# Kernel optimization log

Hardware: AMD Instinct MI355X
Metric: run time of the kernel (lower is better)

Reference implementation:

```python
import jax, jax.numpy as jnp
import numpy as np

TOP_K = 8
N_GROUP = 8
TOPK_GROUP = 4
ROUTED_SCALING_FACTOR = 2.5
NORM_TOPK_PROB = True
TOKENS = 16384
HIDDEN = 4096
N_EXPERTS = 256


def setup_inputs() -> dict:
    key = jax.random.key(0)
    k1, k2, k3 = jax.random.split(key, 3)
    x = jax.random.normal(k1, (TOKENS, HIDDEN), dtype=jnp.float32)
    weight = jax.random.normal(k2, (N_EXPERTS, HIDDEN), dtype=jnp.float32) * 0.02
    e_score_correction_bias = jax.random.normal(k3, (N_EXPERTS,), dtype=jnp.float32) * 0.01
    return {"x": x, "weight": weight, "e_score_correction_bias": e_score_correction_bias}


def reference(x, weight, e_score_correction_bias):
    # gates: [T, E]
    gates = x @ weight.T
    orig_scores = jax.nn.sigmoid(gates.astype(jnp.float32))
    scores = orig_scores + e_score_correction_bias
    T, E = scores.shape
    eg = E // N_GROUP  # experts per group
    s = scores.reshape(T, N_GROUP, eg)
    # group score = sum of top-2 expert scores within each group -> [T, G]
    group_scores = jax.lax.top_k(s, 2)[0].sum(axis=-1)
    # torch code selects the (n_group - topk_group) SMALLEST groups and keeps
    # only those (masked_fill zeroes everything else) -- replicate faithfully.
    k_drop = N_GROUP - TOPK_GROUP
    _, bottom_idx = jax.lax.top_k(-group_scores, k_drop)  # [T, k_drop]
    keep = jnp.zeros((T, N_GROUP), dtype=bool).at[jnp.arange(T)[:, None], bottom_idx].set(True)
    s = jnp.where(keep[:, :, None], s, 0.0).reshape(T, E)
    # torch.topk(-scores) -> indices of the k SMALLEST scores
    _, inds = jax.lax.top_k(-s, TOP_K)  # [T, top_k]
    sel = jnp.take_along_axis(orig_scores, inds, axis=-1)
    if TOP_K > 1 and NORM_TOPK_PROB:
        sel = sel / (sel.sum(axis=-1, keepdims=True) + 1e-20)
    sel = sel * ROUTED_SCALING_FACTOR
    return inds, sel
```

## Files before the change

kernel.cpp:

```cpp
#include <hip/hip_runtime.h>
#include <hip/hip_fp16.h>
#include <cstdint>
#include <cmath>

#define TOKENS  16384
#define HIDDEN  4096
#define NEXP    256
#define TOPK    8
#define KDROP   4

typedef _Float16 f16x8  __attribute__((ext_vector_type(8)));
typedef float    f32x16 __attribute__((ext_vector_type(16)));

#define LO_SCALE 2048.0f
#define LO_INV   (1.0f/2048.0f)

#define WS_G0_OFF 0
#define WS_G1_OFF 16777216
#define WS_WH_OFF 33554432
#define WS_WL_OFF 35651584

__global__ __launch_bounds__(256)
void wsplit(const float* __restrict__ w, _Float16* __restrict__ wh,
            _Float16* __restrict__ wl)
{
    const int idx = blockIdx.x * 256 + threadIdx.x;
    const int e   = idx >> 9;
    const int kg8 = idx & 511;
    const float4* p = (const float4*)(w + (size_t)e * HIDDEN + kg8 * 8);
    float4 f0 = p[0], f1 = p[1];
    float v[8] = {f0.x, f0.y, f0.z, f0.w, f1.x, f1.y, f1.z, f1.w};
    f16x8 hi, lo;
    #pragma unroll
    for (int i = 0; i < 8; ++i) {
        _Float16 h = (_Float16)v[i];
        hi[i] = h;
        lo[i] = (_Float16)((v[i] - (float)h) * LO_SCALE);
    }
    const int kc = kg8 >> 2, s = (kg8 >> 1) & 1, hl = kg8 & 1;
    const int cid = ((kc * 2 + s) * 8 + (e >> 5)) * 64 + hl * 32 + (e & 31);
    ((f16x8*)wh)[cid] = hi;
    ((f16x8*)wl)[cid] = lo;
}

__global__ __launch_bounds__(256, 2)
void gemm_split(const float* __restrict__ x, const _Float16* __restrict__ wh,
                const _Float16* __restrict__ wl,
                float* __restrict__ g0, float* __restrict__ g1)
{
    __shared__ _Float16 Ah[2][64 * 32];
    __shared__ _Float16 Al[2][64 * 32];

    const int tid  = threadIdx.x;
    const int wv   = tid >> 6;
    const int lane = tid & 63;
    const int tok0 = blockIdx.x * 64;
    const int kcg0 = blockIdx.y * 64;
    float* gates_half = blockIdx.y ? g1 : g0;

    const int sm = tid >> 2;
    const int sq = tid & 3;
    const float* xr = x + (size_t)(tok0 + sm) * HIDDEN;
    const int scid = ((sq >> 1) * 2 + (sm >> 5)) * 64 + (sq & 1) * 32 + (sm & 31);

    const f16x8* whc = (const f16x8*)wh;
    const f16x8* wlc = (const f16x8*)wl;

    f32x16 accH[2][2] = {};
    f32x16 accX[2][2] = {};

    f16x8 bh[2][2], bl[2][2];

    {
        const float4* ap = (const float4*)(xr + kcg0 * 32 + sq * 8);
        float4 f0 = ap[0];
        float4 f1 = ap[1];
        #pragma unroll
        for (int s = 0; s < 2; ++s) {
            const int base = ((kcg0 * 2 + s) * 8 + wv * 2) * 64 + lane;
            bh[s][0] = whc[base];
            bh[s][1] = whc[base + 64];
            bl[s][0] = wlc[base];
            bl[s][1] = wlc[base + 64];
        }
        float v[8] = {f0.x, f0.y, f0.z, f0.w, f1.x, f1.y, f1.z, f1.w};
        f16x8 hi, lo;
        #pragma unroll
        for (int i = 0; i < 8; ++i) {
            _Float16 h = (_Float16)v[i];
            hi[i] = h;
            lo[i] = (_Float16)((v[i] - (float)h) * LO_SCALE);
        }
        *(f16x8*)&Ah[0][scid * 8] = hi;
        *(f16x8*)&Al[0][scid * 8] = lo;
    }
    __syncthreads();

    #pragma unroll 2
    for (int kc = 0; kc < 64; ++kc) {
        const int cur  = kc & 1;
        const bool more = (kc < 63);

        float4 a0n, a1n;
        f16x8 bhn[2][2], bln[2][2];
        if (more) {
            const int kcg = kcg0 + kc + 1;
            const float4* ap = (const float4*)(xr + kcg * 32 + sq * 8);
            a0n = ap[0];
            a1n = ap[1];
            #pragma unroll
            for (int s = 0; s < 2; ++s) {
                const int base = ((kcg * 2 + s) * 8 + wv * 2) * 64 + lane;
                bhn[s][0] = whc[base];
                bhn[s][1] = whc[base + 64];
                bln[s][0] = wlc[base];
                bln[s][1] = wlc[base + 64];
            }
        }

        #pragma unroll
        for (int s = 0; s < 2; ++s) {
            f16x8 ah0 = *(const f16x8*)&Ah[cur][((s * 2 + 0) * 64 + lane) * 8];
            f16x8 ah1 = *(const f16x8*)&Ah[cur][((s * 2 + 1) * 64 + lane) * 8];
            f16x8 al0 = *(const f16x8*)&Al[cur][((s * 2 + 0) * 64 + lane) * 8];
            f16x8 al1 = *(const f16x8*)&Al[cur][((s * 2 + 1) * 64 + lane) * 8];

            accH[0][0] = __builtin_amdgcn_mfma_f32_32x32x16_f16(ah0, bh[s][0], accH[0][0], 0, 0, 0);
            accH[0][1] = __builtin_amdgcn_mfma_f32_32x32x16_f16(ah0, bh[s][1], accH[0][1], 0, 0, 0);
            accH[1][0] = __builtin_amdgcn_mfma_f32_32x32x16_f16(ah1, bh[s][0], accH[1][0], 0, 0, 0);
            accH[1][1] = __builtin_amdgcn_mfma_f32_32x32x16_f16(ah1, bh[s][1], accH[1][1], 0, 0, 0);
            accX[0][0] = __builtin_amdgcn_mfma_f32_32x32x16_f16(al0, bh[s][0], accX[0][0], 0, 0, 0);
            accX[0][1] = __builtin_amdgcn_mfma_f32_32x32x16_f16(al0, bh[s][1], accX[0][1], 0, 0, 0);
            accX[1][0] = __builtin_amdgcn_mfma_f32_32x32x16_f16(al1, bh[s][0], accX[1][0], 0, 0, 0);
            accX[1][1] = __builtin_amdgcn_mfma_f32_32x32x16_f16(al1, bh[s][1], accX[1][1], 0, 0, 0);
            accX[0][0] = __builtin_amdgcn_mfma_f32_32x32x16_f16(ah0, bl[s][0], accX[0][0], 0, 0, 0);
            accX[0][1] = __builtin_amdgcn_mfma_f32_32x32x16_f16(ah0, bl[s][1], accX[0][1], 0, 0, 0);
            accX[1][0] = __builtin_amdgcn_mfma_f32_32x32x16_f16(ah1, bl[s][0], accX[1][0], 0, 0, 0);
            accX[1][1] = __builtin_amdgcn_mfma_f32_32x32x16_f16(ah1, bl[s][1], accX[1][1], 0, 0, 0);
        }

        if (more) {
            float v[8] = {a0n.x, a0n.y, a0n.z, a0n.w, a1n.x, a1n.y, a1n.z, a1n.w};
            f16x8 hi, lo;
            #pragma unroll
            for (int i = 0; i < 8; ++i) {
                _Float16 h = (_Float16)v[i];
                hi[i] = h;
                lo[i] = (_Float16)((v[i] - (float)h) * LO_SCALE);
            }
            *(f16x8*)&Ah[cur ^ 1][scid * 8] = hi;
            *(f16x8*)&Al[cur ^ 1][scid * 8] = lo;
            #pragma unroll
            for (int s = 0; s < 2; ++s) {
                bh[s][0] = bhn[s][0]; bh[s][1] = bhn[s][1];
                bl[s][0] = bln[s][0]; bl[s][1] = bln[s][1];
            }
        }
        __syncthreads();
    }

    const int col   = lane & 31;
    const int rbase = 4 * (lane >> 5);
    #pragma unroll
    for (int r = 0; r < 2; ++r)
        #pragma unroll
        for (int c = 0; c < 2; ++c) {
            float* gp = gates_half + (size_t)(tok0 + r * 32) * NEXP + wv * 64 + c * 32 + col;
            #pragma unroll
            for (int reg = 0; reg < 16; ++reg) {
                const int row = (reg & 3) + 8 * (reg >> 2) + rbase;
                gp[(size_t)row * NEXP] = accH[r][c][reg] + accX[r][c][reg] * LO_INV;
            }
        }
}

__device__ __forceinline__ unsigned ordkey(float f) {
    unsigned u = __float_as_uint(f);
    return (u & 0x80000000u) ? ~u : (u | 0x80000000u);
}

__global__ __launch_bounds__(256, 4)
void gate_epilogue(const float* __restrict__ g0,
                   const float* __restrict__ g1,
                   const float* __restrict__ bias,
                   float* __restrict__ out)
{
    const int tid  = threadIdx.x;
    const int wv   = tid >> 6;
    const int lane = tid & 63;
    const int t    = blockIdx.x * 4 + wv;

    float4 ga = ((const float4*)(g0 + (size_t)t * NEXP))[lane];
    float4 gb = ((const float4*)(g1 + (size_t)t * NEXP))[lane];
    float4 bv = ((const float4*)bias)[lane];
    float4 gv = make_float4(ga.x + gb.x, ga.y + gb.y, ga.z + gb.z, ga.w + gb.w);

    float sig0 = 1.0f / (1.0f + expf(-gv.x));
    float sig1 = 1.0f / (1.0f + expf(-gv.y));
    float sig2 = 1.0f / (1.0f + expf(-gv.z));
    float sig3 = 1.0f / (1.0f + expf(-gv.w));
    float sc0 = sig0 + bv.x, sc1 = sig1 + bv.y;
    float sc2 = sig2 + bv.z, sc3 = sig3 + bv.w;

    float m1 = fmaxf(sc0, sc1);
    float m2 = fminf(sc0, sc1);
    if (sc2 > m1) { m2 = m1; m1 = sc2; } else m2 = fmaxf(m2, sc2);
    if (sc3 > m1) { m2 = m1; m1 = sc3; } else m2 = fmaxf(m2, sc3);
    #pragma unroll
    for (int off = 1; off < 8; off <<= 1) {
        float o1 = __shfl_xor(m1, off);
        float o2 = __shfl_xor(m2, off);
        float nm1 = fmaxf(m1, o1);
        float nm2 = fmaxf(fminf(m1, o1), fmaxf(m2, o2));
        m1 = nm1; m2 = nm2;
    }
    float gsum = m1 + m2;
    float gs[8];
    #pragma unroll
    for (int gi = 0; gi < 8; ++gi) gs[gi] = __shfl(gsum, gi * 8);

    int keepmask = 0;
    #pragma unroll
    for (int g = 0; g < 8; ++g) {
        int rank = 0;
        #pragma unroll
        for (int h = 0; h < 8; ++h)
            rank += (gs[h] < gs[g]) || (gs[h] == gs[g] && h < g);
        if (rank < KDROP) keepmask |= (1 << g);
    }
    const bool kept = (keepmask >> (lane >> 3)) & 1;

    const unsigned ib = (unsigned)(lane * 4);
    unsigned long long k0 = ((unsigned long long)ordkey(kept ? sc0 : 0.0f) << 32) | (ib + 0);
    unsigned long long k1 = ((unsigned long long)ordkey(kept ? sc1 : 0.0f) << 32) | (ib + 1);
    unsigned long long k2 = ((unsigned long long)ordkey(kept ? sc2 : 0.0f) << 32) | (ib + 2);
    unsigned long long k3 = ((unsigned long long)ordkey(kept ? sc3 : 0.0f) << 32) | (ib + 3);

    float ssum = 0.0f, myval = 0.0f;
    int myidx = 0;
    #pragma unroll
    for (int r = 0; r < TOPK; ++r) {
        unsigned long long kmin = k0 < k1 ? k0 : k1;
        if (k2 < kmin) kmin = k2;
        if (k3 < kmin) kmin = k3;
        #pragma unroll
        for (int off = 32; off >= 1; off >>= 1) {
            unsigned long long o = __shfl_xor(kmin, off);
            if (o < kmin) kmin = o;
        }
        const int id   = (int)(kmin & 0xffffffffull);
        const int src  = id >> 2;
        const int slot = id & 3;
        float vsrc = (slot == 0) ? sig0 : (slot == 1) ? sig1
                   : (slot == 2) ? sig2 : sig3;
        float v = __shfl(vsrc, src);
        ssum += v;
        if (lane == r) { myidx = id; myval = v; }
        const bool mine = (lane == src);
        if (mine && slot == 0) k0 = ~0ull;
        if (mine && slot == 1) k1 = ~0ull;
        if (mine && slot == 2) k2 = ~0ull;
        if (mine && slot == 3) k3 = ~0ull;
    }

    if (lane < TOPK) {
        out[(size_t)t * TOPK + lane] = (float)myidx;
        out[(size_t)TOKENS * TOPK + (size_t)t * TOPK + lane] =
            myval / (ssum + 1e-20f) * 2.5f;
    }
}

extern "C" void kernel_launch(void* const* d_in, const int* in_sizes, int n_in,
                              void* d_out, int out_size, void* d_ws, size_t ws_size,
                              hipStream_t stream)
{
    const float* x    = (const float*)d_in[0];
    const float* w    = (const float*)d_in[1];
    const float* bias = (const float*)d_in[2];
    float* out = (float*)d_out;

    float*     g0 = (float*)((char*)d_ws + WS_G0_OFF);
    float*     g1 = (float*)((char*)d_ws + WS_G1_OFF);
    _Float16*  wh = (_Float16*)((char*)d_ws + WS_WH_OFF);
    _Float16*  wl = (_Float16*)((char*)d_ws + WS_WL_OFF);

    wsplit<<<dim3(512), dim3(256), 0, stream>>>(w, wh, wl);
    gemm_split<<<dim3(TOKENS / 64, 2), dim3(256), 0, stream>>>(x, wh, wl, g0, g1);
    gate_epilogue<<<dim3(TOKENS / 4), dim3(256), 0, stream>>>(g0, g1, bias, out);
}
```

Before: 429.2 us.

## Use 512-thread GEMM blocks covering 128 tokens, sharing B fragments, with two-stage A prefetch

Each GEMM block now runs 8 waves covering 128 tokens, split as two 64-token halves. Both halves share the same per-wave weight fragments, so each block reads the B operand once for twice the tokens. The x rows are prefetched two k-steps ahead in registers to hide global latency, and the grid becomes 1D with 256 blocks. In exchange, more registers are needed per thread under launch_bounds(512,2), and the grid has fewer blocks than before, which lowers occupancy and load-balancing slack.

```diff
diff --git a/kernel.cpp b/kernel.cpp
--- a/kernel.cpp
+++ b/kernel.cpp
@@ -11,6 +11,7 @@
 
 typedef _Float16 f16x8  __attribute__((ext_vector_type(8)));
 typedef float    f32x16 __attribute__((ext_vector_type(16)));
+typedef float    f32x4  __attribute__((ext_vector_type(4)));
 
 #define LO_SCALE 2048.0f
 #define LO_INV   (1.0f/2048.0f)
@@ -43,24 +44,31 @@
     ((f16x8*)wl)[cid] = lo;
 }
 
-__global__ __launch_bounds__(256, 2)
+__global__ __launch_bounds__(512, 2)
 void gemm_split(const float* __restrict__ x, const _Float16* __restrict__ wh,
                 const _Float16* __restrict__ wl,
                 float* __restrict__ g0, float* __restrict__ g1)
 {
-    __shared__ _Float16 Ah[2][64 * 32];
-    __shared__ _Float16 Al[2][64 * 32];
+    __shared__ _Float16 Ah[2][2][64 * 32];
+    __shared__ _Float16 Al[2][2][64 * 32];
 
     const int tid  = threadIdx.x;
-    const int wv   = tid >> 6;
+    const int w    = tid >> 6;
     const int lane = tid & 63;
-    const int tok0 = blockIdx.x * 64;
-    const int kcg0 = blockIdx.y * 64;
-    float* gates_half = blockIdx.y ? g1 : g0;
-
-    const int sm = tid >> 2;
-    const int sq = tid & 3;
-    const float* xr = x + (size_t)(tok0 + sm) * HIDDEN;
+    const int th   = w >> 2;
+    const int wq   = w & 3;
+
+    const int bid  = blockIdx.x;
+    const int y    = bid & 1;
+    const int tok0 = (bid >> 1) * 128;
+    const int kcg0 = y * 64;
+    float* gates_half = y ? g1 : g0;
+
+    const int stok = tid >> 2;
+    const int sq   = tid & 3;
+    const int sth  = stok >> 6;
+    const int sm   = stok & 63;
+    const float* xr = x + (size_t)(tok0 + stok) * HIDDEN + (size_t)kcg0 * 32 + sq * 8;
     const int scid = ((sq >> 1) * 2 + (sm >> 5)) * 64 + (sq & 1) * 32 + (sm & 31);
 
     const f16x8* whc = (const f16x8*)wh;
@@ -70,14 +78,16 @@
     f32x16 accX[2][2] = {};
 
     f16x8 bh[2][2], bl[2][2];
+    f32x4 aM0, aM1;
 
     {
-        const float4* ap = (const float4*)(xr + kcg0 * 32 + sq * 8);
-        float4 f0 = ap[0];
-        float4 f1 = ap[1];
+        f32x4 f0 = *(const f32x4*)(xr);
+        f32x4 f1 = *(const f32x4*)(xr + 4);
+        aM0 = *(const f32x4*)(xr + 32);
+        aM1 = *(const f32x4*)(xr + 36);
         #pragma unroll
         for (int s = 0; s < 2; ++s) {
-            const int base = ((kcg0 * 2 + s) * 8 + wv * 2) * 64 + lane;
+            const int base = ((kcg0 * 2 + s) * 8 + wq * 2) * 64 + lane;
             bh[s][0] = whc[base];
             bh[s][1] = whc[base + 64];
             bl[s][0] = wlc[base];
@@ -91,26 +101,27 @@
             hi[i] = h;
             lo[i] = (_Float16)((v[i] - (float)h) * LO_SCALE);
         }
-        *(f16x8*)&Ah[0][scid * 8] = hi;
-        *(f16x8*)&Al[0][scid * 8] = lo;
+        *(f16x8*)&Ah[0][sth][scid * 8] = hi;
+        *(f16x8*)&Al[0][sth][scid * 8] = lo;
     }
     __syncthreads();
 
     #pragma unroll 2
     for (int kc = 0; kc < 64; ++kc) {
-        const int cur  = kc & 1;
-        const bool more = (kc < 63);
-
-        float4 a0n, a1n;
+        const int cur = kc & 1;
+
+        f32x4 aN0, aN1;
         f16x8 bhn[2][2], bln[2][2];
-        if (more) {
+        if (kc + 2 < 64) {
+            const float* ap = xr + (kc + 2) * 32;
+            aN0 = *(const f32x4*)(ap);
+            aN1 = *(const f32x4*)(ap + 4);
+        }
+        if (kc + 1 < 64) {
             const int kcg = kcg0 + kc + 1;
-            const float4* ap = (const float4*)(xr + kcg * 32 + sq * 8);
-            a0n = ap[0];
-            a1n = ap[1];
             #pragma unroll
             for (int s = 0; s < 2; ++s) {
-                const int base = ((kcg * 2 + s) * 8 + wv * 2) * 64 + lane;
+                const int base = ((kcg * 2 + s) * 8 + wq * 2) * 64 + lane;
                 bhn[s][0] = whc[base];
                 bhn[s][1] = whc[base + 64];
                 bln[s][0] = wlc[base];
@@ -120,10 +131,10 @@
 
         #pragma unroll
         for (int s = 0; s < 2; ++s) {
-            f16x8 ah0 = *(const f16x8*)&Ah[cur][((s * 2 + 0) * 64 + lane) * 8];
-            f16x8 ah1 = *(const f16x8*)&Ah[cur][((s * 2 + 1) * 64 + lane) * 8];
-            f16x8 al0 = *(const f16x8*)&Al[cur][((s * 2 + 0) * 64 + lane) * 8];
-            f16x8 al1 = *(const f16x8*)&Al[cur][((s * 2 + 1) * 64 + lane) * 8];
+            f16x8 ah0 = *(const f16x8*)&Ah[cur][th][((s * 2 + 0) * 64 + lane) * 8];
+            f16x8 ah1 = *(const f16x8*)&Ah[cur][th][((s * 2 + 1) * 64 + lane) * 8];
+            f16x8 al0 = *(const f16x8*)&Al[cur][th][((s * 2 + 0) * 64 + lane) * 8];
+            f16x8 al1 = *(const f16x8*)&Al[cur][th][((s * 2 + 1) * 64 + lane) * 8];
 
             accH[0][0] = __builtin_amdgcn_mfma_f32_32x32x16_f16(ah0, bh[s][0], accH[0][0], 0, 0, 0);
             accH[0][1] = __builtin_amdgcn_mfma_f32_32x32x16_f16(ah0, bh[s][1], accH[0][1], 0, 0, 0);
@@ -139,8 +150,8 @@
             accX[1][1] = __builtin_amdgcn_mfma_f32_32x32x16_f16(ah1, bl[s][1], accX[1][1], 0, 0, 0);
         }
 
-        if (more) {
-            float v[8] = {a0n.x, a0n.y, a0n.z, a0n.w, a1n.x, a1n.y, a1n.z, a1n.w};
+        if (kc + 1 < 64) {
+            float v[8] = {aM0.x, aM0.y, aM0.z, aM0.w, aM1.x, aM1.y, aM1.z, aM1.w};
             f16x8 hi, lo;
             #pragma unroll
             for (int i = 0; i < 8; ++i) {
@@ -148,8 +159,9 @@
                 hi[i] = h;
                 lo[i] = (_Float16)((v[i] - (float)h) * LO_SCALE);
             }
-            *(f16x8*)&Ah[cur ^ 1][scid * 8] = hi;
-            *(f16x8*)&Al[cur ^ 1][scid * 8] = lo;
+            *(f16x8*)&Ah[cur ^ 1][sth][scid * 8] = hi;
+            *(f16x8*)&Al[cur ^ 1][sth][scid * 8] = lo;
+            aM0 = aN0; aM1 = aN1;
             #pragma unroll
             for (int s = 0; s < 2; ++s) {
                 bh[s][0] = bhn[s][0]; bh[s][1] = bhn[s][1];
@@ -165,7 +177,8 @@
     for (int r = 0; r < 2; ++r)
         #pragma unroll
         for (int c = 0; c < 2; ++c) {
-            float* gp = gates_half + (size_t)(tok0 + r * 32) * NEXP + wv * 64 + c * 32 + col;
+            float* gp = gates_half + (size_t)(tok0 + th * 64 + r * 32) * NEXP
+                      + wq * 64 + c * 32 + col;
             #pragma unroll
             for (int reg = 0; reg < 16; ++reg) {
                 const int row = (reg & 3) + 8 * (reg >> 2) + rbase;
@@ -285,6 +298,6 @@
     _Float16*  wl = (_Float16*)((char*)d_ws + WS_WL_OFF);
 
     wsplit<<<dim3(512), dim3(256), 0, stream>>>(w, wh, wl);
-    gemm_split<<<dim3(TOKENS / 64, 2), dim3(256), 0, stream>>>(x, wh, wl, g0, g1);
+    gemm_split<<<dim3(256), dim3(512), 0, stream>>>(x, wh, wl, g0, g1);
     gate_epilogue<<<dim3(TOKENS / 4), dim3(256), 0, stream>>>(g0, g1, bias, out);
 }
```

Measured after the change: 440.1 us. +2.5%, slower.

## Use 8 waves per GEMM block with one 32-expert column each and deeper x prefetch

Applied to the files above, without the earlier changes.

The split-fp16 gate GEMM block grows from 4 to 8 waves, so each wave now owns a 64x32 output tile (2 accumulator pairs) instead of 64x64. Each thread stages only 4 x-values per k-chunk, and x loads are prefetched two chunks ahead. The grid is flattened, with the K-half taken from the low bit of the block index. The aim is more waves for latency hiding, higher occupancy from fewer accumulator registers, and deeper global-load pipelining. The cost is that each B fragment is reused half as much per wave, so LDS reads of A per MFMA double.

```diff
diff --git a/kernel.cpp b/kernel.cpp
--- a/kernel.cpp
+++ b/kernel.cpp
@@ -10,7 +10,9 @@
 #define KDROP   4
 
 typedef _Float16 f16x8  __attribute__((ext_vector_type(8)));
+typedef _Float16 f16x4  __attribute__((ext_vector_type(4)));
 typedef float    f32x16 __attribute__((ext_vector_type(16)));
+typedef float    f32x4  __attribute__((ext_vector_type(4)));
 
 #define LO_SCALE 2048.0f
 #define LO_INV   (1.0f/2048.0f)
@@ -43,7 +45,7 @@
     ((f16x8*)wl)[cid] = lo;
 }
 
-__global__ __launch_bounds__(256, 2)
+__global__ __launch_bounds__(512, 4)
 void gemm_split(const float* __restrict__ x, const _Float16* __restrict__ wh,
                 const _Float16* __restrict__ wl,
                 float* __restrict__ g0, float* __restrict__ g1)
@@ -52,69 +54,67 @@
     __shared__ _Float16 Al[2][64 * 32];
 
     const int tid  = threadIdx.x;
-    const int wv   = tid >> 6;
+    const int w    = tid >> 6;
     const int lane = tid & 63;
-    const int tok0 = blockIdx.x * 64;
-    const int kcg0 = blockIdx.y * 64;
-    float* gates_half = blockIdx.y ? g1 : g0;
-
-    const int sm = tid >> 2;
-    const int sq = tid & 3;
-    const float* xr = x + (size_t)(tok0 + sm) * HIDDEN;
-    const int scid = ((sq >> 1) * 2 + (sm >> 5)) * 64 + (sq & 1) * 32 + (sm & 31);
+
+    const int bid  = blockIdx.x;
+    const int y    = bid & 1;
+    const int tok0 = (bid >> 1) * 64;
+    const int kcg0 = y * 64;
+    float* gates_half = y ? g1 : g0;
+
+    const int srow = (tid >> 1) & 31;
+    const int shl  = (tid >> 6) & 1;
+    const int sr   = (tid >> 7) & 1;
+    const int ss   = (tid >> 8) & 1;
+    const int stok = sr * 32 + srow;
+    const int sk   = ss * 16 + shl * 8 + (tid & 1) * 4;
+    const float* xr = x + (size_t)(tok0 + stok) * HIDDEN + (size_t)kcg0 * 32 + sk;
 
     const f16x8* whc = (const f16x8*)wh;
     const f16x8* wlc = (const f16x8*)wl;
 
-    f32x16 accH[2][2] = {};
-    f32x16 accX[2][2] = {};
-
-    f16x8 bh[2][2], bl[2][2];
+    f32x16 accH[2] = {};
+    f32x16 accX[2] = {};
+
+    f16x8 bh[2], bl[2];
+    f32x4 aM;
 
     {
-        const float4* ap = (const float4*)(xr + kcg0 * 32 + sq * 8);
-        float4 f0 = ap[0];
-        float4 f1 = ap[1];
+        f32x4 a0 = *(const f32x4*)(xr);
+        aM = *(const f32x4*)(xr + 32);
         #pragma unroll
         for (int s = 0; s < 2; ++s) {
-            const int base = ((kcg0 * 2 + s) * 8 + wv * 2) * 64 + lane;
-            bh[s][0] = whc[base];
-            bh[s][1] = whc[base + 64];
-            bl[s][0] = wlc[base];
-            bl[s][1] = wlc[base + 64];
-        }
-        float v[8] = {f0.x, f0.y, f0.z, f0.w, f1.x, f1.y, f1.z, f1.w};
-        f16x8 hi, lo;
-        #pragma unroll
-        for (int i = 0; i < 8; ++i) {
-            _Float16 h = (_Float16)v[i];
+            bh[s] = whc[((kcg0 * 2 + s) * 8 + w) * 64 + lane];
+            bl[s] = wlc[((kcg0 * 2 + s) * 8 + w) * 64 + lane];
+        }
+        f16x4 hi, lo;
+        #pragma unroll
+        for (int i = 0; i < 4; ++i) {
+            _Float16 h = (_Float16)a0[i];
             hi[i] = h;
-            lo[i] = (_Float16)((v[i] - (float)h) * LO_SCALE);
-        }
-        *(f16x8*)&Ah[0][scid * 8] = hi;
-        *(f16x8*)&Al[0][scid * 8] = lo;
+            lo[i] = (_Float16)((a0[i] - (float)h) * LO_SCALE);
+        }
+        *(f16x4*)&Ah[0][tid * 4] = hi;
+        *(f16x4*)&Al[0][tid * 4] = lo;
     }
     __syncthreads();
 
     #pragma unroll 2
     for (int kc = 0; kc < 64; ++kc) {
-        const int cur  = kc & 1;
-        const bool more = (kc < 63);
-
-        float4 a0n, a1n;
-        f16x8 bhn[2][2], bln[2][2];
-        if (more) {
+        const int cur = kc & 1;
+
+        f32x4 aN;
+        f16x8 bhn[2], bln[2];
+        if (kc + 2 < 64) {
+            aN = *(const f32x4*)(xr + (kc + 2) * 32);
+        }
+        if (kc + 1 < 64) {
             const int kcg = kcg0 + kc + 1;
-            const float4* ap = (const float4*)(xr + kcg * 32 + sq * 8);
-            a0n = ap[0];
-            a1n = ap[1];
             #pragma unroll
             for (int s = 0; s < 2; ++s) {
-                const int base = ((kcg * 2 + s) * 8 + wv * 2) * 64 + lane;
-                bhn[s][0] = whc[base];
-                bhn[s][1] = whc[base + 64];
-                bln[s][0] = wlc[base];
-                bln[s][1] = wlc[base + 64];
+                bhn[s] = whc[((kcg * 2 + s) * 8 + w) * 64 + lane];
+                bln[s] = wlc[((kcg * 2 + s) * 8 + w) * 64 + lane];
             }
         }
 
@@ -125,35 +125,29 @@
             f16x8 al0 = *(const f16x8*)&Al[cur][((s * 2 + 0) * 64 + lane) * 8];
             f16x8 al1 = *(const f16x8*)&Al[cur][((s * 2 + 1) * 64 + lane) * 8];
 
-            accH[0][0] = __builtin_amdgcn_mfma_f32_32x32x16_f16(ah0, bh[s][0], accH[0][0], 0, 0, 0);
-            accH[0][1] = __builtin_amdgcn_mfma_f32_32x32x16_f16(ah0, bh[s][1], accH[0][1], 0, 0, 0);
-            accH[1][0] = __builtin_amdgcn_mfma_f32_32x32x16_f16(ah1, bh[s][0], accH[1][0], 0, 0, 0);
-            accH[1][1] = __builtin_amdgcn_mfma_f32_32x32x16_f16(ah1, bh[s][1], accH[1][1], 0, 0, 0);
-            accX[0][0] = __builtin_amdgcn_mfma_f32_32x32x16_f16(al0, bh[s][0], accX[0][0], 0, 0, 0);
-            accX[0][1] = __builtin_amdgcn_mfma_f32_32x32x16_f16(al0, bh[s][1], accX[0][1], 0, 0, 0);
-            accX[1][0] = __builtin_amdgcn_mfma_f32_32x32x16_f16(al1, bh[s][0], accX[1][0], 0, 0, 0);
-            accX[1][1] = __builtin_amdgcn_mfma_f32_32x32x16_f16(al1, bh[s][1], accX[1][1], 0, 0, 0);
-            accX[0][0] = __builtin_amdgcn_mfma_f32_32x32x16_f16(ah0, bl[s][0], accX[0][0], 0, 0, 0);
-            accX[0][1] = __builtin_amdgcn_mfma_f32_32x32x16_f16(ah0, bl[s][1], accX[0][1], 0, 0, 0);
-            accX[1][0] = __builtin_amdgcn_mfma_f32_32x32x16_f16(ah1, bl[s][0], accX[1][0], 0, 0, 0);
-            accX[1][1] = __builtin_amdgcn_mfma_f32_32x32x16_f16(ah1, bl[s][1], accX[1][1], 0, 0, 0);
-        }
-
-        if (more) {
-            float v[8] = {a0n.x, a0n.y, a0n.z, a0n.w, a1n.x, a1n.y, a1n.z, a1n.w};
-            f16x8 hi, lo;
+            accH[0] = __builtin_amdgcn_mfma_f32_32x32x16_f16(ah0, bh[s], accH[0], 0, 0, 0);
+            accH[1] = __builtin_amdgcn_mfma_f32_32x32x16_f16(ah1, bh[s], accH[1], 0, 0, 0);
+            accX[0] = __builtin_amdgcn_mfma_f32_32x32x16_f16(al0, bh[s], accX[0], 0, 0, 0);
+            accX[1] = __builtin_amdgcn_mfma_f32_32x32x16_f16(al1, bh[s], accX[1], 0, 0, 0);
+            accX[0] = __builtin_amdgcn_mfma_f32_32x32x16_f16(ah0, bl[s], accX[0], 0, 0, 0);
+            accX[1] = __builtin_amdgcn_mfma_f32_32x32x16_f16(ah1, bl[s], accX[1], 0, 0, 0);
+        }
+
+        if (kc + 1 < 64) {
+            f16x4 hi, lo;
             #pragma unroll
-            for (int i = 0; i < 8; ++i) {
-                _Float16 h = (_Float16)v[i];
+            for (int i = 0; i < 4; ++i) {
+                _Float16 h = (_Float16)aM[i];
                 hi[i] = h;
-                lo[i] = (_Float16)((v[i] - (float)h) * LO_SCALE);
+                lo[i] = (_Float16)((aM[i] - (float)h) * LO_SCALE);
             }
-            *(f16x8*)&Ah[cur ^ 1][scid * 8] = hi;
-            *(f16x8*)&Al[cur ^ 1][scid * 8] = lo;
+            *(f16x4*)&Ah[cur ^ 1][tid * 4] = hi;
+            *(f16x4*)&Al[cur ^ 1][tid * 4] = lo;
+            aM = aN;
             #pragma unroll
             for (int s = 0; s < 2; ++s) {
-                bh[s][0] = bhn[s][0]; bh[s][1] = bhn[s][1];
-                bl[s][0] = bln[s][0]; bl[s][1] = bln[s][1];
+                bh[s] = bhn[s];
+                bl[s] = bln[s];
             }
         }
         __syncthreads();
@@ -162,16 +156,14 @@
     const int col   = lane & 31;
     const int rbase = 4 * (lane >> 5);
     #pragma unroll
-    for (int r = 0; r < 2; ++r)
-        #pragma unroll
-        for (int c = 0; c < 2; ++c) {
-            float* gp = gates_half + (size_t)(tok0 + r * 32) * NEXP + wv * 64 + c * 32 + col;
-            #pragma unroll
-            for (int reg = 0; reg < 16; ++reg) {
-                const int row = (reg & 3) + 8 * (reg >> 2) + rbase;
-                gp[(size_t)row * NEXP] = accH[r][c][reg] + accX[r][c][reg] * LO_INV;
-            }
-        }
+    for (int r = 0; r < 2; ++r) {
+        float* gp = gates_half + (size_t)(tok0 + r * 32) * NEXP + w * 32 + col;
+        #pragma unroll
+        for (int reg = 0; reg < 16; ++reg) {
+            const int row = (reg & 3) + 8 * (reg >> 2) + rbase;
+            gp[(size_t)row * NEXP] = accH[r][reg] + accX[r][reg] * LO_INV;
+        }
+    }
 }
 
 __device__ __forceinline__ unsigned ordkey(float f) {
@@ -285,6 +277,6 @@
     _Float16*  wl = (_Float16*)((char*)d_ws + WS_WL_OFF);
 
     wsplit<<<dim3(512), dim3(256), 0, stream>>>(w, wh, wl);
-    gemm_split<<<dim3(TOKENS / 64, 2), dim3(256), 0, stream>>>(x, wh, wl, g0, g1);
+    gemm_split<<<dim3(512), dim3(512), 0, stream>>>(x, wh, wl, g0, g1);
     gate_epilogue<<<dim3(TOKENS / 4), dim3(256), 0, stream>>>(g0, g1, bias, out);
 }
```

Result: slower. 481.2 us (+12.1%).
